# Kernel optimization log

Measured on AMD Instinct MI355X. Metric: run time of the kernel, lower is better.

## Reference

```python
import jax, jax.numpy as jnp
import numpy as np

# ---- static config matching init_kwargs / input_specs ----
B, H, W_IN, IN_CAPS, ATOMS = 2, 48, 48, 8, 16
KER, STRIDE, OUT_CAPS, ROUTINGS = 3, 1, 16, 3


def setup_inputs() -> dict:
    key = jax.random.key(0)
    k1, k2 = jax.random.split(key)
    x = jax.random.normal(k1, (B, H, W_IN, IN_CAPS * (ATOMS + 1)), dtype=jnp.float32)
    # W: [input_num_capsule, num_capsule, 4, 4], he_normal-ish scale (fan_in=16)
    W = jax.random.normal(k2, (IN_CAPS, OUT_CAPS, 4, 4), dtype=jnp.float32) * np.float32((2.0 / 16.0) ** 0.5)
    return {"input_tensor": x, "W": W}


def _kernel_tile(x, k=KER, stride=STRIDE):
    # Equivalent to the depthwise-conv patch-extraction trick + transpose:
    # output [B, Ho, Wo, k*k, C]
    b, h, w, c = x.shape
    ho = (h - k) // stride + 1
    wo = (w - k) // stride + 1
    patches = jnp.stack(
        [x[:, i:i + stride * ho:stride, j:j + stride * wo:stride, :]
         for i in range(k) for j in range(k)],
        axis=3,
    )
    return patches


def _squash(s, eps=1e-7):
    sq = jnp.sum(s * s, axis=-1, keepdims=True)
    return (sq / (1.0 + sq)) * s / jnp.sqrt(sq + eps)


def reference(input_tensor, W):
    t = _kernel_tile(input_tensor)                      # [B,Ho,Wo,kk,C]
    b, ho, wo, kk, c = t.shape
    n = b * ho * wo
    t = t.reshape(n, kk * IN_CAPS, ATOMS + 1)           # [N, kk*in_caps, 17]
    pose = t[..., :ATOMS].reshape(n, kk, IN_CAPS, 4, 4)
    act = t[..., ATOMS].reshape(n, kk * IN_CAPS)        # input capsule activations
    # vote transform: pose @ W per (input capsule -> output capsule)
    votes = jnp.einsum('nkiab,iobc->nkioac', pose, W)
    votes = votes.reshape(n, kk * IN_CAPS, OUT_CAPS, ATOMS)  # [N, kkin, out, 16]
    # iterative routing-by-agreement, weighted by input activation
    logits = jnp.zeros((n, kk * IN_CAPS, OUT_CAPS), dtype=votes.dtype)
    v = None
    for r in range(ROUTINGS):
        coup = jax.nn.softmax(logits, axis=2) * act[:, :, None]
        s = jnp.einsum('nko,nkoe->noe', coup, votes)    # weighted vote sum
        v = _squash(s)                                  # [N, out, 16]
        if r < ROUTINGS - 1:
            logits = logits + jnp.einsum('nkoe,noe->nko', votes, v)
    return v.reshape(b, ho, wo, OUT_CAPS, ATOMS)
```

## Files before the change

### kernel.cpp

```cpp
#include <hip/hip_runtime.h>


#define IN_CAPS 8
#define OUT_CAPS 16
#define KK 9
#define KKIN 72
#define BATCH 2
#define H_IN 48
#define W_IN 48
#define HO 46
#define WO 46
#define CIN 136
#define NPIX (BATCH*HO*WO)

typedef float v2f __attribute__((ext_vector_type(2)));
typedef float v4f __attribute__((ext_vector_type(4)));

__device__ __forceinline__ v2f lo2(v4f v) { return __builtin_shufflevector(v, v, 0, 1); }
__device__ __forceinline__ v2f hi2(v4f v) { return __builtin_shufflevector(v, v, 2, 3); }
__device__ __forceinline__ v2f fma2(v2f a, v2f b, v2f c) {
    return __builtin_elementwise_fma(a, b, c);
}

template<int CTRL>
__device__ __forceinline__ float dpp_f(float x) {
    return __int_as_float(
        __builtin_amdgcn_update_dpp(0, __float_as_int(x), CTRL, 0xF, 0xF, true));
}
__device__ __forceinline__ float row_sum16(float x) {
    x += dpp_f<0xB1>(x);
    x += dpp_f<0x4E>(x);
    x += dpp_f<0x124>(x);
    x += dpp_f<0x128>(x);
    return x;
}

__device__ __forceinline__ int pose_row(int k) {
    return k * 20 + ((k >> 3) & 1) * 4;
}
__device__ __forceinline__ int g_row(int o, int ic) {
    return (o * 8 + ic) * 20 + o * 4;
}

__global__ __launch_bounds__(256, 4)
void capsule_routing_kernel(const float* __restrict__ x,
                            const float* __restrict__ Wg,
                            float* __restrict__ out)
{
    __shared__ alignas(16) float pose_s[1440];
    __shared__ alignas(16) float pose_t[16 * 76];
    __shared__ float act_s[KKIN];
    __shared__ alignas(16) float g_s[2620];
    __shared__ alignas(16) float coup_s[OUT_CAPS * 76];

    const int tid = threadIdx.x;
    const int o = tid >> 4;
    const int e = tid & 15;
    const int c = e & 3;

    const int n   = blockIdx.x;
    const int b   = n / (HO * WO);
    const int rem = n - b * (HO * WO);
    const int ho  = rem / WO;
    const int wo  = rem - ho * WO;

    v2f w01[IN_CAPS], w23[IN_CAPS];
    #pragma unroll
    for (int i = 0; i < IN_CAPS; ++i) {
        const v4f wv = *reinterpret_cast<const v4f*>(
            &Wg[((i * OUT_CAPS + o) * 4 + c) * 4]);
        w01[i] = lo2(wv);
        w23[i] = hi2(wv);
    }

    for (int idx = tid; idx < KK * CIN; idx += 256) {
        int p  = idx / CIN;
        int cc = idx - p * CIN;
        int py = p / 3, px = p - py * 3;
        float val = x[(((b * H_IN + ho + py) * W_IN) + (wo + px)) * CIN + cc];
        int ic = cc / 17;
        int aa = cc - ic * 17;
        int k  = p * IN_CAPS + ic;
        if (aa == 16) {
            act_s[k] = val;
        } else {
            pose_s[pose_row(k) + aa] = val;
            pose_t[aa * 76 + k] = val;
        }
    }
    __syncthreads();

    if (tid < KKIN) {
        float cv = act_s[tid] * 0.0625f;
        #pragma unroll
        for (int j = 0; j < OUT_CAPS; ++j) coup_s[j * 76 + tid] = cv;
    }
    __syncthreads();

    const int kf  = tid >> 1;
    const int hf  = tid & 1;
    const int ick = kf & 7;
    float lreg8[8] = {0.f,0.f,0.f,0.f,0.f,0.f,0.f,0.f};

    const v4f* cp = reinterpret_cast<const v4f*>(&coup_s[o * 76]);
    const v4f* pp = reinterpret_cast<const v4f*>(&pose_t[e * 76]);

    float v = 0.f;
    #pragma unroll 1
    for (int r = 0; r < 3; ++r) {
        v2f M01 = {0.f,0.f}, M23 = {0.f,0.f}, M45 = {0.f,0.f}, M67 = {0.f,0.f};
        #pragma unroll
        for (int p = 0; p < KK; ++p) {
            const v4f c0 = cp[2*p], c1 = cp[2*p+1];
            const v4f q0 = pp[2*p], q1 = pp[2*p+1];
            M01 = fma2(lo2(c0), lo2(q0), M01);
            M23 = fma2(hi2(c0), hi2(q0), M23);
            M45 = fma2(lo2(c1), lo2(q1), M45);
            M67 = fma2(hi2(c1), hi2(q1), M67);
        }
        const float Mc[8] = {M01.x, M01.y, M23.x, M23.y,
                             M45.x, M45.y, M67.x, M67.y};
        v2f U01 = {0.f,0.f}, U23 = {0.f,0.f};
        #pragma unroll
        for (int ic = 0; ic < 8; ++ic) {
            const v2f mm = {Mc[ic], Mc[ic]};
            U01 = fma2(w01[ic], mm, U01);
            U23 = fma2(w23[ic], mm, U23);
        }
        float Z0 = U01.x, Z1 = U01.y, Z2 = U23.x, Z3 = U23.y;
        Z0 += dpp_f<0xB1>(Z0); Z1 += dpp_f<0xB1>(Z1);
        Z2 += dpp_f<0xB1>(Z2); Z3 += dpp_f<0xB1>(Z3);
        Z0 += dpp_f<0x4E>(Z0); Z1 += dpp_f<0x4E>(Z1);
        Z2 += dpp_f<0x4E>(Z2); Z3 += dpp_f<0x4E>(Z3);
        const float s = (c == 0) ? Z0 : (c == 1) ? Z1 : (c == 2) ? Z2 : Z3;

        const float sq = row_sum16(s * s);
        v = s * (sq / ((1.f + sq) * sqrtf(sq + 1e-7f)));

        if (r < 2) {
            const float vq0 = dpp_f<0x00>(v);
            const float vq1 = dpp_f<0x55>(v);
            const float vq2 = dpp_f<0xAA>(v);
            const float vq3 = dpp_f<0xFF>(v);
            const v2f vq01 = {vq0, vq1};
            const v2f vq23 = {vq2, vq3};
            #pragma unroll
            for (int ic = 0; ic < 8; ++ic) {
                v2f h = fma2(w23[ic], vq23, w01[ic] * vq01);
                g_s[g_row(o, ic) + e] = h.x + h.y;
            }
            __syncthreads();
            if (tid < 2 * KKIN) {
                const v4f* pk = reinterpret_cast<const v4f*>(
                    &pose_s[pose_row(kf)]);
                const v4f p0 = pk[0], p1 = pk[1], p2 = pk[2], p3 = pk[3];
                const v2f q0 = lo2(p0), q1 = hi2(p0), q2 = lo2(p1), q3 = hi2(p1);
                const v2f q4 = lo2(p2), q5 = hi2(p2), q6 = lo2(p3), q7 = hi2(p3);
                float lg[8];
                #pragma unroll
                for (int j = 0; j < 8; ++j) {
                    const int oo = hf * 8 + j;
                    const v4f* gp = reinterpret_cast<const v4f*>(
                        &g_s[g_row(oo, ick)]);
                    const v4f g0 = gp[0], g1 = gp[1], g2 = gp[2], g3 = gp[3];
                    v2f A = fma2(q2, lo2(g1), fma2(q4, lo2(g2),
                              fma2(q6, lo2(g3), q0 * lo2(g0))));
                    v2f Bv = fma2(q3, hi2(g1), fma2(q5, hi2(g2),
                              fma2(q7, hi2(g3), q1 * hi2(g0))));
                    lreg8[j] += (A.x + A.y) + (Bv.x + Bv.y);
                    lg[j] = lreg8[j];
                }
                float mx = -1e30f;
                #pragma unroll
                for (int j = 0; j < 8; ++j) mx = fmaxf(mx, lg[j]);
                mx = fmaxf(mx, dpp_f<0xB1>(mx));
                float sum = 0.f;
                #pragma unroll
                for (int j = 0; j < 8; ++j) { lg[j] = __expf(lg[j] - mx); sum += lg[j]; }
                sum += dpp_f<0xB1>(sum);
                const float scale = act_s[kf] / sum;
                #pragma unroll
                for (int j = 0; j < 8; ++j)
                    coup_s[(hf * 8 + j) * 76 + kf] = lg[j] * scale;
            }
            __syncthreads();
        }
    }

    out[n * 256 + tid] = v;
}

extern "C" void kernel_launch(void* const* d_in, const int* in_sizes, int n_in,
                              void* d_out, int out_size, void* d_ws, size_t ws_size,
                              hipStream_t stream) {
    const float* x  = (const float*)d_in[0];
    const float* Wt = (const float*)d_in[1];
    float* outp = (float*)d_out;
    capsule_routing_kernel<<<dim3(NPIX), dim3(256), 0, stream>>>(x, Wt, outp);
}
```

Measured before the change: 92.58 us.

## Process two pixels per block to amortize weight loads and barriers

Each block now handles two output pixels instead of one, with doubled shared-memory buffers and per-pixel register state. Weight registers and the __syncthreads barriers are shared across both pixels, and the two pixels' independent work can interleave to hide latency. The cost is roughly double the LDS per block, a lowered occupancy target in launch bounds (3 blocks instead of 4), and half as many blocks (4232 → 2116). NPIX is even, so the grid covers every pixel.

```diff
diff --git a/kernel.cpp b/kernel.cpp
--- a/kernel.cpp
+++ b/kernel.cpp
@@ -42,27 +42,26 @@
     return (o * 8 + ic) * 20 + o * 4;
 }
 
-__global__ __launch_bounds__(256, 4)
+#define PSZ  1440
+#define PTSZ 1216
+#define GSZ  2620
+#define CSZ  1216
+
+__global__ __launch_bounds__(256, 3)
 void capsule_routing_kernel(const float* __restrict__ x,
                             const float* __restrict__ Wg,
                             float* __restrict__ out)
 {
-    __shared__ alignas(16) float pose_s[1440];
-    __shared__ alignas(16) float pose_t[16 * 76];
-    __shared__ float act_s[KKIN];
-    __shared__ alignas(16) float g_s[2620];
-    __shared__ alignas(16) float coup_s[OUT_CAPS * 76];
+    __shared__ alignas(16) float pose_s[2 * PSZ];
+    __shared__ alignas(16) float pose_t[2 * PTSZ];
+    __shared__ float act_s[2 * KKIN];
+    __shared__ alignas(16) float g_s[2 * GSZ];
+    __shared__ alignas(16) float coup_s[2 * CSZ];
 
     const int tid = threadIdx.x;
     const int o = tid >> 4;
     const int e = tid & 15;
     const int c = e & 3;
-
-    const int n   = blockIdx.x;
-    const int b   = n / (HO * WO);
-    const int rem = n - b * (HO * WO);
-    const int ho  = rem / WO;
-    const int wo  = rem - ho * WO;
 
     v2f w01[IN_CAPS], w23[IN_CAPS];
     #pragma unroll
@@ -73,121 +72,141 @@
         w23[i] = hi2(wv);
     }
 
-    for (int idx = tid; idx < KK * CIN; idx += 256) {
-        int p  = idx / CIN;
-        int cc = idx - p * CIN;
-        int py = p / 3, px = p - py * 3;
-        float val = x[(((b * H_IN + ho + py) * W_IN) + (wo + px)) * CIN + cc];
-        int ic = cc / 17;
-        int aa = cc - ic * 17;
-        int k  = p * IN_CAPS + ic;
-        if (aa == 16) {
-            act_s[k] = val;
-        } else {
-            pose_s[pose_row(k) + aa] = val;
-            pose_t[aa * 76 + k] = val;
+    #pragma unroll
+    for (int pix = 0; pix < 2; ++pix) {
+        const int n   = blockIdx.x * 2 + pix;
+        const int b   = n / (HO * WO);
+        const int rem = n - b * (HO * WO);
+        const int ho  = rem / WO;
+        const int wo  = rem - ho * WO;
+        float* ps = &pose_s[pix * PSZ];
+        float* pt = &pose_t[pix * PTSZ];
+        float* as = &act_s[pix * KKIN];
+        for (int idx = tid; idx < KK * CIN; idx += 256) {
+            int p  = idx / CIN;
+            int cc = idx - p * CIN;
+            int py = p / 3, px = p - py * 3;
+            float val = x[(((b * H_IN + ho + py) * W_IN) + (wo + px)) * CIN + cc];
+            int ic = cc / 17;
+            int aa = cc - ic * 17;
+            int k  = p * IN_CAPS + ic;
+            if (aa == 16) as[k] = val;
+            else { ps[pose_row(k) + aa] = val; pt[aa * 76 + k] = val; }
         }
     }
     __syncthreads();
 
     if (tid < KKIN) {
-        float cv = act_s[tid] * 0.0625f;
         #pragma unroll
-        for (int j = 0; j < OUT_CAPS; ++j) coup_s[j * 76 + tid] = cv;
+        for (int pix = 0; pix < 2; ++pix) {
+            float cv = act_s[pix * KKIN + tid] * 0.0625f;
+            #pragma unroll
+            for (int j = 0; j < OUT_CAPS; ++j)
+                coup_s[pix * CSZ + j * 76 + tid] = cv;
+        }
     }
     __syncthreads();
 
     const int kf  = tid >> 1;
     const int hf  = tid & 1;
     const int ick = kf & 7;
-    float lreg8[8] = {0.f,0.f,0.f,0.f,0.f,0.f,0.f,0.f};
-
-    const v4f* cp = reinterpret_cast<const v4f*>(&coup_s[o * 76]);
-    const v4f* pp = reinterpret_cast<const v4f*>(&pose_t[e * 76]);
-
-    float v = 0.f;
+    float lreg8[2][8] = {{0.f,0.f,0.f,0.f,0.f,0.f,0.f,0.f},
+                         {0.f,0.f,0.f,0.f,0.f,0.f,0.f,0.f}};
+
+    float v[2] = {0.f, 0.f};
     #pragma unroll 1
     for (int r = 0; r < 3; ++r) {
-        v2f M01 = {0.f,0.f}, M23 = {0.f,0.f}, M45 = {0.f,0.f}, M67 = {0.f,0.f};
         #pragma unroll
-        for (int p = 0; p < KK; ++p) {
-            const v4f c0 = cp[2*p], c1 = cp[2*p+1];
-            const v4f q0 = pp[2*p], q1 = pp[2*p+1];
-            M01 = fma2(lo2(c0), lo2(q0), M01);
-            M23 = fma2(hi2(c0), hi2(q0), M23);
-            M45 = fma2(lo2(c1), lo2(q1), M45);
-            M67 = fma2(hi2(c1), hi2(q1), M67);
-        }
-        const float Mc[8] = {M01.x, M01.y, M23.x, M23.y,
-                             M45.x, M45.y, M67.x, M67.y};
-        v2f U01 = {0.f,0.f}, U23 = {0.f,0.f};
-        #pragma unroll
-        for (int ic = 0; ic < 8; ++ic) {
-            const v2f mm = {Mc[ic], Mc[ic]};
-            U01 = fma2(w01[ic], mm, U01);
-            U23 = fma2(w23[ic], mm, U23);
-        }
-        float Z0 = U01.x, Z1 = U01.y, Z2 = U23.x, Z3 = U23.y;
-        Z0 += dpp_f<0xB1>(Z0); Z1 += dpp_f<0xB1>(Z1);
-        Z2 += dpp_f<0xB1>(Z2); Z3 += dpp_f<0xB1>(Z3);
-        Z0 += dpp_f<0x4E>(Z0); Z1 += dpp_f<0x4E>(Z1);
-        Z2 += dpp_f<0x4E>(Z2); Z3 += dpp_f<0x4E>(Z3);
-        const float s = (c == 0) ? Z0 : (c == 1) ? Z1 : (c == 2) ? Z2 : Z3;
-
-        const float sq = row_sum16(s * s);
-        v = s * (sq / ((1.f + sq) * sqrtf(sq + 1e-7f)));
+        for (int pix = 0; pix < 2; ++pix) {
+            const v4f* cp = reinterpret_cast<const v4f*>(&coup_s[pix * CSZ + o * 76]);
+            const v4f* pp = reinterpret_cast<const v4f*>(&pose_t[pix * PTSZ + e * 76]);
+            v2f M01 = {0.f,0.f}, M23 = {0.f,0.f}, M45 = {0.f,0.f}, M67 = {0.f,0.f};
+            #pragma unroll
+            for (int p = 0; p < KK; ++p) {
+                const v4f c0 = cp[2*p], c1 = cp[2*p+1];
+                const v4f q0 = pp[2*p], q1 = pp[2*p+1];
+                M01 = fma2(lo2(c0), lo2(q0), M01);
+                M23 = fma2(hi2(c0), hi2(q0), M23);
+                M45 = fma2(lo2(c1), lo2(q1), M45);
+                M67 = fma2(hi2(c1), hi2(q1), M67);
+            }
+            const float Mc[8] = {M01.x, M01.y, M23.x, M23.y,
+                                 M45.x, M45.y, M67.x, M67.y};
+            v2f U01 = {0.f,0.f}, U23 = {0.f,0.f};
+            #pragma unroll
+            for (int ic = 0; ic < 8; ++ic) {
+                const v2f mm = {Mc[ic], Mc[ic]};
+                U01 = fma2(w01[ic], mm, U01);
+                U23 = fma2(w23[ic], mm, U23);
+            }
+            float Z0 = U01.x, Z1 = U01.y, Z2 = U23.x, Z3 = U23.y;
+            Z0 += dpp_f<0xB1>(Z0); Z1 += dpp_f<0xB1>(Z1);
+            Z2 += dpp_f<0xB1>(Z2); Z3 += dpp_f<0xB1>(Z3);
+            Z0 += dpp_f<0x4E>(Z0); Z1 += dpp_f<0x4E>(Z1);
+            Z2 += dpp_f<0x4E>(Z2); Z3 += dpp_f<0x4E>(Z3);
+            const float s = (c == 0) ? Z0 : (c == 1) ? Z1 : (c == 2) ? Z2 : Z3;
+            const float sq = row_sum16(s * s);
+            v[pix] = s * (sq / ((1.f + sq) * sqrtf(sq + 1e-7f)));
+        }
 
         if (r < 2) {
-            const float vq0 = dpp_f<0x00>(v);
-            const float vq1 = dpp_f<0x55>(v);
-            const float vq2 = dpp_f<0xAA>(v);
-            const float vq3 = dpp_f<0xFF>(v);
-            const v2f vq01 = {vq0, vq1};
-            const v2f vq23 = {vq2, vq3};
-            #pragma unroll
-            for (int ic = 0; ic < 8; ++ic) {
-                v2f h = fma2(w23[ic], vq23, w01[ic] * vq01);
-                g_s[g_row(o, ic) + e] = h.x + h.y;
+            #pragma unroll
+            for (int pix = 0; pix < 2; ++pix) {
+                const float vq0 = dpp_f<0x00>(v[pix]);
+                const float vq1 = dpp_f<0x55>(v[pix]);
+                const float vq2 = dpp_f<0xAA>(v[pix]);
+                const float vq3 = dpp_f<0xFF>(v[pix]);
+                const v2f vq01 = {vq0, vq1};
+                const v2f vq23 = {vq2, vq3};
+                #pragma unroll
+                for (int ic = 0; ic < 8; ++ic) {
+                    v2f h = fma2(w23[ic], vq23, w01[ic] * vq01);
+                    g_s[pix * GSZ + g_row(o, ic) + e] = h.x + h.y;
+                }
             }
             __syncthreads();
             if (tid < 2 * KKIN) {
-                const v4f* pk = reinterpret_cast<const v4f*>(
-                    &pose_s[pose_row(kf)]);
-                const v4f p0 = pk[0], p1 = pk[1], p2 = pk[2], p3 = pk[3];
-                const v2f q0 = lo2(p0), q1 = hi2(p0), q2 = lo2(p1), q3 = hi2(p1);
-                const v2f q4 = lo2(p2), q5 = hi2(p2), q6 = lo2(p3), q7 = hi2(p3);
-                float lg[8];
                 #pragma unroll
-                for (int j = 0; j < 8; ++j) {
-                    const int oo = hf * 8 + j;
-                    const v4f* gp = reinterpret_cast<const v4f*>(
-                        &g_s[g_row(oo, ick)]);
-                    const v4f g0 = gp[0], g1 = gp[1], g2 = gp[2], g3 = gp[3];
-                    v2f A = fma2(q2, lo2(g1), fma2(q4, lo2(g2),
-                              fma2(q6, lo2(g3), q0 * lo2(g0))));
-                    v2f Bv = fma2(q3, hi2(g1), fma2(q5, hi2(g2),
-                              fma2(q7, hi2(g3), q1 * hi2(g0))));
-                    lreg8[j] += (A.x + A.y) + (Bv.x + Bv.y);
-                    lg[j] = lreg8[j];
+                for (int pix = 0; pix < 2; ++pix) {
+                    const v4f* pk = reinterpret_cast<const v4f*>(
+                        &pose_s[pix * PSZ + pose_row(kf)]);
+                    const v4f p0 = pk[0], p1 = pk[1], p2 = pk[2], p3 = pk[3];
+                    const v2f q0 = lo2(p0), q1 = hi2(p0), q2 = lo2(p1), q3 = hi2(p1);
+                    const v2f q4 = lo2(p2), q5 = hi2(p2), q6 = lo2(p3), q7 = hi2(p3);
+                    float lg[8];
+                    #pragma unroll
+                    for (int j = 0; j < 8; ++j) {
+                        const int oo = hf * 8 + j;
+                        const v4f* gp = reinterpret_cast<const v4f*>(
+                            &g_s[pix * GSZ + g_row(oo, ick)]);
+                        const v4f g0 = gp[0], g1 = gp[1], g2 = gp[2], g3 = gp[3];
+                        v2f A  = fma2(q2, lo2(g1), fma2(q4, lo2(g2),
+                                  fma2(q6, lo2(g3), q0 * lo2(g0))));
+                        v2f Bv = fma2(q3, hi2(g1), fma2(q5, hi2(g2),
+                                  fma2(q7, hi2(g3), q1 * hi2(g0))));
+                        lreg8[pix][j] += (A.x + A.y) + (Bv.x + Bv.y);
+                        lg[j] = lreg8[pix][j];
+                    }
+                    float mx = -1e30f;
+                    #pragma unroll
+                    for (int j = 0; j < 8; ++j) mx = fmaxf(mx, lg[j]);
+                    mx = fmaxf(mx, dpp_f<0xB1>(mx));
+                    float sum = 0.f;
+                    #pragma unroll
+                    for (int j = 0; j < 8; ++j) { lg[j] = __expf(lg[j] - mx); sum += lg[j]; }
+                    sum += dpp_f<0xB1>(sum);
+                    const float scale = act_s[pix * KKIN + kf] / sum;
+                    #pragma unroll
+                    for (int j = 0; j < 8; ++j)
+                        coup_s[pix * CSZ + (hf * 8 + j) * 76 + kf] = lg[j] * scale;
                 }
-                float mx = -1e30f;
-                #pragma unroll
-                for (int j = 0; j < 8; ++j) mx = fmaxf(mx, lg[j]);
-                mx = fmaxf(mx, dpp_f<0xB1>(mx));
-                float sum = 0.f;
-                #pragma unroll
-                for (int j = 0; j < 8; ++j) { lg[j] = __expf(lg[j] - mx); sum += lg[j]; }
-                sum += dpp_f<0xB1>(sum);
-                const float scale = act_s[kf] / sum;
-                #pragma unroll
-                for (int j = 0; j < 8; ++j)
-                    coup_s[(hf * 8 + j) * 76 + kf] = lg[j] * scale;
             }
             __syncthreads();
         }
     }
 
-    out[n * 256 + tid] = v;
+    out[(blockIdx.x * 2 + 0) * 256 + tid] = v[0];
+    out[(blockIdx.x * 2 + 1) * 256 + tid] = v[1];
 }
 
 extern "C" void kernel_launch(void* const* d_in, const int* in_sizes, int n_in,
@@ -196,5 +215,5 @@
     const float* x  = (const float*)d_in[0];
     const float* Wt = (const float*)d_in[1];
     float* outp = (float*)d_out;
-    capsule_routing_kernel<<<dim3(NPIX), dim3(256), 0, stream>>>(x, Wt, outp);
-}
+    capsule_routing_kernel<<<dim3(NPIX / 2), dim3(256), 0, stream>>>(x, Wt, outp);
+}
```

Measured after the change: 97.19 us. 5.0% more time.
